# Performance work log

Hardware: AMD Instinct MI355X
Metric: run time of the kernel (lower is better)

The kernel has to match this reference:

```python
import jax, jax.numpy as jnp
import numpy as np

DIM = 2048
H = 16
DK = DIM // H   # head_k = 128
DV = DIM // H   # head_v = 128
B = 4
N = 4096
INV_SQRT_DK = 1.0 / float(np.sqrt(DK))


def setup_inputs() -> dict:
    key = jax.random.key(0)
    ks = jax.random.split(key, 12)
    s = 0.02
    return {
        "x": jax.random.normal(ks[0], (B, N, DIM), dtype=jnp.float32),
        "M_fast_prev": jax.random.normal(ks[1], (B, H, DK, DV), dtype=jnp.float32) * 0.05,
        "M_slow_prev": jax.random.normal(ks[2], (B, H, DK, DV), dtype=jnp.float32) * 0.05,
        "Wq": jax.random.normal(ks[3], (DIM, H * DK), dtype=jnp.float32) * s,
        "Wk": jax.random.normal(ks[4], (DIM, H * DK), dtype=jnp.float32) * s,
        "Wv": jax.random.normal(ks[5], (DIM, H * DV), dtype=jnp.float32) * s,
        "Wo": jax.random.normal(ks[6], (H * DV, DIM), dtype=jnp.float32) * s,
        "W_bilinear": jax.random.normal(ks[7], (H, DK, DK), dtype=jnp.float32) * 0.02,
        "fast_slope": jnp.full((H, 1, 1), 0.5, dtype=jnp.float32),
        "slow_slope": jnp.full((H, 1, 1), 0.01, dtype=jnp.float32),
        "inter_fast": jnp.full((H, 1, 1), 0.1, dtype=jnp.float32),
        "inter_slow": jnp.full((H, 1, 1), 0.9, dtype=jnp.float32),
        "S_fast": jax.random.normal(ks[8], (H, DK, DK), dtype=jnp.float32) * 0.05,
        "S_slow": jax.random.normal(ks[9], (H, DK, DK), dtype=jnp.float32) * 0.02,
        "f1_w": jax.random.normal(ks[10], (DIM, DIM // 2), dtype=jnp.float32) * s,
        "f1_b": jnp.zeros((DIM // 2,), dtype=jnp.float32),
        "f2_w": jax.random.normal(ks[11], (DIM // 2, H), dtype=jnp.float32) * s,
        "f2_b": jnp.zeros((H,), dtype=jnp.float32),
    }


def reference(x, M_fast_prev, M_slow_prev, Wq, Wk, Wv, Wo, W_bilinear,
              fast_slope, slow_slope, inter_fast, inter_slow,
              S_fast, S_slow, f1_w, f1_b, f2_w, f2_b):
    b, n, _ = x.shape
    # projections -> [b, h, n, d]
    q = (x @ Wq).reshape(b, n, H, DK).transpose(0, 2, 1, 3)
    k = (x @ Wk).reshape(b, n, H, DK).transpose(0, 2, 1, 3)
    v = (x @ Wv).reshape(b, n, H, DV).transpose(0, 2, 1, 3)

    # bilinear resonance modulation of keys
    resonance = jnp.tanh(jnp.einsum('bhnd,hde->bhne', k, W_bilinear))
    k_mod = k * (1.0 + 0.5 * resonance) * INV_SQRT_DK

    # exponential fast/slow decay weights over positions: [h, n, 1]
    idx = (jnp.arange(n, dtype=x.dtype) - (n - 1))[:, None]  # [n, 1]
    fast_w = jnp.exp(fast_slope * idx)  # [h, n, 1]
    slow_w = jnp.exp(slow_slope * idx)

    k_fast = k_mod * fast_w[None]  # [b, h, n, dk]
    k_slow = k_mod * slow_w[None]

    # outer-product state accumulation: [b, h, dk, dv]
    M_fast_curr = jnp.einsum('bhnd,bhnv->bhdv', k_fast, v)
    M_slow_curr = jnp.einsum('bhnd,bhnv->bhdv', k_slow, v)

    # inter-block state carry
    M_fast = M_fast_prev * inter_fast[None] + M_fast_curr
    M_slow = M_slow_prev * inter_slow[None] + M_slow_curr

    # refinement: (I + S) @ M
    eye = jnp.eye(DK, dtype=x.dtype)
    Mf_ref = jnp.einsum('hde,bhev->bhdv', eye[None] + S_fast, M_fast)
    Ms_ref = jnp.einsum('hde,bhev->bhdv', eye[None] + S_slow, M_slow)

    o_fast = jnp.einsum('bhnd,bhdv->bhnv', q, Mf_ref)
    o_slow = jnp.einsum('bhnd,bhdv->bhnv', q, Ms_ref)

    # flux gating from pooled tokens
    h1 = jax.nn.silu(x.mean(axis=1) @ f1_w + f1_b)
    psi = jax.nn.sigmoid(h1 @ f2_w + f2_b)  # [b, h]
    pe = psi[:, :, None, None]

    o_blend = (1.0 - pe) * o_fast + pe * o_slow  # [b, h, n, dv]
    o_blend = o_blend.transpose(0, 2, 1, 3).reshape(b, n, H * DV)
    out = o_blend @ Wo
    return out, M_fast, M_slow, psi
```

## Files before the change

kernel.cpp:

```cpp
#include <hip/hip_runtime.h>
#include <math.h>

typedef __bf16 bf16;
typedef __attribute__((ext_vector_type(8))) __bf16 bf16x8;
typedef __attribute__((ext_vector_type(4))) __bf16 bf16x4;
typedef __attribute__((ext_vector_type(2))) __bf16 bf16x2;
typedef __attribute__((ext_vector_type(4))) float f32x4;

#define DIM 2048
#define NH 16
#define DKK 128
#define BATCH 4
#define SEQ 4096
#define BN (BATCH*SEQ)
#define INV_SQRT_DK 0.08838834764831845f

#define MFMA16(a,b,c) __builtin_amdgcn_mfma_f32_16x16x32_bf16((a),(b),(c),0,0,0)

#define GLDS(gp, lp) __builtin_amdgcn_global_load_lds( \
    (const __attribute__((address_space(1))) void*)(gp), \
    (__attribute__((address_space(3))) void*)(lp), 16, 0, 0)

__device__ inline void stage_tile(const bf16* __restrict__ g, int ld,
                                  bf16* lds, int lane, int wave) {
  const int rl = lane >> 3;
  const int gc = ((lane & 7) ^ (rl & 7)) << 3;
  const bf16* gp = g + (size_t)(wave * 32 + rl) * ld + gc;
#pragma unroll
  for (int t = 0; t < 4; ++t)
    GLDS(gp + (size_t)(t * 8) * ld, lds + (wave * 32 + t * 8) * 64);
}

__device__ inline bf16x8 frag8(const bf16* lds, int r, int kc) {
  return *(const bf16x8*)(lds + r * 64 + (((kc ^ (r & 7)) << 3)));
}

__device__ inline int sq64(int r, int c) {
  return r * 64 + ((((c >> 3) ^ (r & 7)) << 3) | (c & 7));
}

__device__ inline float fast_exp(float x) { return __expf(x); }
__device__ inline float fast_tanh(float x) {
  float e2 = __expf(2.f * x);
  return 1.f - 2.f / (e2 + 1.f);
}

__global__ __launch_bounds__(256) void conv_bf16(const float* __restrict__ x,
                                                 bf16* __restrict__ y) {
  int i = (blockIdx.x * 256 + threadIdx.x) * 4;
  float4 v = *(const float4*)(x + i);
  bf16x4 o = { (bf16)v.x, (bf16)v.y, (bf16)v.z, (bf16)v.w };
  *(bf16x4*)(y + i) = o;
}

__global__ __launch_bounds__(256) void tconv3(const float* W0, const float* W1,
                                              const float* W2,
                                              bf16* O0, bf16* O1, bf16* O2) {
  __shared__ float tile[32][33];
  const float* Wp; bf16* Op;
  switch (blockIdx.z) {
    case 0: Wp = W0; Op = O0; break;
    case 1: Wp = W1; Op = O1; break;
    default: Wp = W2; Op = O2; break;
  }
  int c0 = blockIdx.x * 32, r0 = blockIdx.y * 32;
  int tx = threadIdx.x, ty = threadIdx.y;
#pragma unroll
  for (int i = 0; i < 4; ++i)
    tile[ty + i*8][tx] = Wp[(size_t)(r0 + ty + i*8) * DIM + c0 + tx];
  __syncthreads();
#pragma unroll
  for (int i = 0; i < 4; ++i)
    Op[(size_t)(c0 + ty + i*8) * DIM + r0 + tx] = (bf16)tile[tx][ty + i*8];
}

__global__ __launch_bounds__(256) void tconvWb(const float* __restrict__ W,
                                               bf16* __restrict__ Wt) {
  __shared__ float tile[32][33];
  const float* Wp = W + (size_t)blockIdx.z * DKK * DKK;
  bf16* Wtp = Wt + (size_t)blockIdx.z * DKK * DKK;
  int c0 = blockIdx.x * 32, r0 = blockIdx.y * 32;
  int tx = threadIdx.x, ty = threadIdx.y;
#pragma unroll
  for (int i = 0; i < 4; ++i)
    tile[ty + i*8][tx] = Wp[(size_t)(r0 + ty + i*8) * DKK + c0 + tx];
  __syncthreads();
#pragma unroll
  for (int i = 0; i < 4; ++i)
    Wtp[(size_t)(c0 + ty + i*8) * DKK + r0 + tx] = (bf16)tile[tx][ty + i*8];
}

__global__ __launch_bounds__(256) void rweights(const float* __restrict__ fs,
                                                const float* __restrict__ ss,
                                                float* __restrict__ rbuf) {
  int n = blockIdx.x * 256 + threadIdx.x;
  int h = blockIdx.y;
  rbuf[h * SEQ + n] = fast_exp((fs[h] - ss[h]) * (float)(n - (SEQ - 1)));
}

__global__ void zero_f32(float* p, int n) {
  int i = blockIdx.x * 256 + threadIdx.x;
  if (i < n) p[i] = 0.f;
}

__global__ __launch_bounds__(256) void mean_part(const bf16* __restrict__ xb,
                                                 float* __restrict__ xm) {
  int d0 = (blockIdx.x * 256 + threadIdx.x) * 2;
  int b = blockIdx.z;
  const bf16* xp = xb + ((size_t)b * SEQ + (size_t)blockIdx.y * 256) * DIM + d0;
  float s0 = 0.f, s1 = 0.f;
#pragma unroll 8
  for (int n = 0; n < 256; ++n) {
    bf16x2 v = *(const bf16x2*)(xp + (size_t)n * DIM);
    s0 += (float)v[0]; s1 += (float)v[1];
  }
  atomicAdd(&xm[b * DIM + d0], s0);
  atomicAdd(&xm[b * DIM + d0 + 1], s1);
}

__global__ __launch_bounds__(256) void mlp1(const float* __restrict__ xm,
                                            const float* __restrict__ f1w,
                                            float* __restrict__ h1raw) {
  int j = blockIdx.x * 256 + threadIdx.x;
  int b = blockIdx.y;
  int k0 = blockIdx.z * 256;
  const float* xmb = xm + b * DIM + k0;
  const float* w = f1w + (size_t)k0 * (DIM/2) + j;
  float s = 0.f;
#pragma unroll 4
  for (int k = 0; k < 256; ++k) s += xmb[k] * w[(size_t)k * (DIM/2)];
  atomicAdd(&h1raw[b * (DIM/2) + j], s);
}

__global__ void mlp2(const float* __restrict__ h1raw,
                     const float* __restrict__ f1b,
                     const float* __restrict__ f2w,
                     const float* __restrict__ f2b,
                     float* __restrict__ psi_out) {
  int t = threadIdx.x;
  int b = t >> 4, h = t & 15;
  float s = f2b[h];
  for (int k = 0; k < DIM/2; ++k) {
    float hv = h1raw[b * (DIM/2) + k] * (1.f / (float)SEQ) + f1b[k];
    hv = hv / (1.f + fast_exp(-hv));
    s += hv * f2w[k * NH + h];
  }
  psi_out[t] = 1.f / (1.f + fast_exp(-s));
}

template<int MODE>
__global__ __launch_bounds__(512, 2) void gemm256(const bf16* __restrict__ A, int lda,
                                                  const bf16* __restrict__ Bt, int ldb,
                                                  void* __restrict__ Cv, int ldc, int K) {
  __shared__ bf16 smem[65536];
  const int tid = threadIdx.x;
  const int lane = tid & 63;
  const int wave = tid >> 6;
  const int quad = lane >> 4;
  const int l15 = lane & 15;
  const int wm = (wave >> 2) * 128;
  const int wn = (wave & 3) * 64;
  const size_t m0 = (size_t)blockIdx.y * 256;
  const size_t n0 = (size_t)blockIdx.x * 256;
  const bf16* Ap = A;
  const bf16* Bp = Bt;
  size_t mrow = m0;
  size_t cbat = 0;
  if (MODE == 3) Bp += (size_t)(m0 >> 12) * DIM * DIM;
  if (MODE == 4) {
    size_t b = m0 >> 11;
    Ap += b * (size_t)DIM * DIM;
    cbat = b * (size_t)DIM * DIM;
    mrow = m0 & 2047;
  }
  const bf16* Arow = Ap + mrow * (size_t)lda;
  const bf16* Brow = Bp + n0 * (size_t)ldb;
  f32x4 acc[8][4] = {};
  const int NT = K >> 6;
  stage_tile(Arow, lda, smem, lane, wave);
  stage_tile(Brow, ldb, smem + 32768, lane, wave);
  for (int kt = 0; kt < NT; ++kt) {
    const int cur = kt & 1;
    const bf16* sA = smem + cur * 16384;
    const bf16* sB = smem + 32768 + cur * 16384;
    if (kt + 1 < NT) {
      const int nxt = cur ^ 1;
      const int k0 = (kt + 1) << 6;
      stage_tile(Arow + k0, lda, smem + nxt * 16384, lane, wave);
      stage_tile(Brow + k0, ldb, smem + 32768 + nxt * 16384, lane, wave);
      asm volatile("s_waitcnt vmcnt(8)\n\ts_barrier" ::: "memory");
    } else {
      asm volatile("s_waitcnt vmcnt(0)\n\ts_barrier" ::: "memory");
    }
    bf16x8 bfr[2][4];
#pragma unroll
    for (int kk = 0; kk < 2; ++kk)
#pragma unroll
      for (int j = 0; j < 4; ++j)
        bfr[kk][j] = frag8(sB, wn + j * 16 + l15, kk * 4 + quad);
#pragma unroll
    for (int i2 = 0; i2 < 4; ++i2) {
      bf16x8 af[2][2];
#pragma unroll
      for (int ii = 0; ii < 2; ++ii)
#pragma unroll
        for (int kk = 0; kk < 2; ++kk)
          af[ii][kk] = frag8(sA, wm + (i2 * 2 + ii) * 16 + l15, kk * 4 + quad);
      __builtin_amdgcn_s_setprio(1);
#pragma unroll
      for (int ii = 0; ii < 2; ++ii)
#pragma unroll
        for (int j = 0; j < 4; ++j) {
          acc[i2*2+ii][j] = MFMA16(af[ii][0], bfr[0][j], acc[i2*2+ii][j]);
          acc[i2*2+ii][j] = MFMA16(af[ii][1], bfr[1][j], acc[i2*2+ii][j]);
        }
      __builtin_amdgcn_s_setprio(0);
    }
    asm volatile("s_barrier" ::: "memory");
  }
  if (MODE == 2) {
    const int bb = (int)(m0 >> 12);
    const int nb0 = (int)(m0 & 4095) + wm + quad * 4;
    bf16* vt = (bf16*)Cv;
#pragma unroll
    for (int i = 0; i < 8; ++i)
#pragma unroll
      for (int j = 0; j < 4; ++j) {
        int colg = (int)n0 + wn + j * 16 + l15;
        int h = colg >> 7, dv = colg & 127;
        bf16x4 p = { (bf16)acc[i][j][0], (bf16)acc[i][j][1],
                     (bf16)acc[i][j][2], (bf16)acc[i][j][3] };
        *(bf16x4*)(vt + ((size_t)(bb * NH + h) * DKK + dv) * SEQ + nb0 + i * 16) = p;
      }
  } else {
#pragma unroll
    for (int i = 0; i < 8; ++i)
#pragma unroll
      for (int j = 0; j < 4; ++j) {
        size_t col = n0 + wn + j * 16 + l15;
        size_t row = mrow + wm + i * 16 + quad * 4;
#pragma unroll
        for (int r = 0; r < 4; ++r) {
          if (MODE == 3) ((float*)Cv)[(row + r) * ldc + col] = acc[i][j][r];
          else           ((bf16*)Cv)[cbat + (row + r) * ldc + col] = (bf16)acc[i][j][r];
        }
      }
  }
}

__global__ __launch_bounds__(256) void res_fuse(const bf16* __restrict__ kn,
                                                const bf16* __restrict__ Wbt,
                                                const float* __restrict__ slow_slope,
                                                bf16* __restrict__ kts) {
  __shared__ bf16 sA2[2][8192];
  __shared__ bf16 sB[8192];
  const int tid = threadIdx.x;
  const int lane = tid & 63;
  const int wave = tid >> 6;
  const int quad = lane >> 4;
  const int l15 = lane & 15;
  const int wm = (wave & 1) * 64;
  const int wn = (wave >> 1) * 64;
  const int nt = blockIdx.x;
  const int bh = blockIdx.y;
  const int h = bh & (NH - 1), b = bh >> 4;
  const bf16* Ap = kn + ((size_t)b * SEQ + (size_t)nt * 128) * DIM + h * DKK;
  const bf16* Bp = Wbt + (size_t)h * DKK * DKK;
  const float ss = slow_slope[h];
  f32x4 acc[4][4] = {};
#pragma unroll
  for (int c = 0; c < 2; ++c) {
    stage_tile(Ap + c * 64, DIM, sA2[c], lane, wave);
    stage_tile(Bp + c * 64, DKK, sB, lane, wave);
    __syncthreads();
#pragma unroll
    for (int kk = 0; kk < 2; ++kk) {
      const int kc = kk * 4 + quad;
      bf16x8 af[4], bfr[4];
#pragma unroll
      for (int i = 0; i < 4; ++i) af[i] = frag8(sA2[c], wm + i*16 + l15, kc);
#pragma unroll
      for (int j = 0; j < 4; ++j) bfr[j] = frag8(sB, wn + j*16 + l15, kc);
#pragma unroll
      for (int i = 0; i < 4; ++i)
#pragma unroll
        for (int j = 0; j < 4; ++j)
          acc[i][j] = MFMA16(af[i], bfr[j], acc[i][j]);
    }
    __syncthreads();
  }
  float wsv[4][4];
#pragma unroll
  for (int i = 0; i < 4; ++i)
#pragma unroll
    for (int r = 0; r < 4; ++r) {
      int ng = nt * 128 + wm + i*16 + quad*4 + r;
      wsv[i][r] = fast_exp(ss * (float)(ng - (SEQ - 1)));
    }
#pragma unroll
  for (int i = 0; i < 4; ++i)
#pragma unroll
    for (int j = 0; j < 4; ++j) {
      int e = wn + j*16 + l15;
      const bf16* sAe = sA2[e >> 6];
      int ec = e & 63;
      bf16x4 p;
#pragma unroll
      for (int r = 0; r < 4; ++r) {
        int nl = wm + i*16 + quad*4 + r;
        float kv = (float)sAe[sq64(nl, ec)];
        float res = fast_tanh(acc[i][j][r]);
        p[r] = (bf16)(kv * (1.f + 0.5f * res) * INV_SQRT_DK * wsv[i][r]);
      }
      *(bf16x4*)(kts + ((size_t)bh * DKK + e) * SEQ + nt * 128 + wm + i*16 + quad*4) = p;
    }
}

__global__ __launch_bounds__(256) void mcurr(const bf16* __restrict__ kts,
                                             const bf16* __restrict__ vt,
                                             const float* __restrict__ rbuf,
                                             float* __restrict__ partials) {
  __shared__ bf16 sK[128 * 64];
  __shared__ bf16 sV[128 * 64];
  const int tid = threadIdx.x;
  const int lane = tid & 63;
  const int wave = tid >> 6;
  const int quad = lane >> 4;
  const int wm = (wave & 1) * 64, wn = (wave >> 1) * 64;
  const int s = blockIdx.x;
  const int bh = blockIdx.y;
  const int h = bh & (NH - 1);
  const bf16* Ap = kts + (size_t)bh * DKK * SEQ;
  const bf16* Bp = vt + (size_t)bh * DKK * SEQ;
  const float* rp = rbuf + (size_t)h * SEQ;
  f32x4 accF[4][4] = {}, accS[4][4] = {};
  for (int k0 = s * 512; k0 < s * 512 + 512; k0 += 64) {
    stage_tile(Ap + k0, SEQ, sK, lane, wave);
    stage_tile(Bp + k0, SEQ, sV, lane, wave);
    __syncthreads();
#pragma unroll
    for (int kk = 0; kk < 2; ++kk) {
      const int kc = kk * 4 + quad;
      const int kn_ = k0 + kc * 8;
      float rv[8];
      *(f32x4*)rv       = *(const f32x4*)(rp + kn_);
      *(f32x4*)(rv + 4) = *(const f32x4*)(rp + kn_ + 4);
      bf16x8 afS[4], afF[4], bfv[4];
#pragma unroll
      for (int i = 0; i < 4; ++i) afS[i] = frag8(sK, wm + i*16 + (lane & 15), kc);
#pragma unroll
      for (int j = 0; j < 4; ++j) bfv[j] = frag8(sV, wn + j*16 + (lane & 15), kc);
#pragma unroll
      for (int i = 0; i < 4; ++i)
#pragma unroll
        for (int e = 0; e < 8; ++e)
          afF[i][e] = (bf16)((float)afS[i][e] * rv[e]);
#pragma unroll
      for (int i = 0; i < 4; ++i)
#pragma unroll
        for (int j = 0; j < 4; ++j) {
          accS[i][j] = MFMA16(afS[i], bfv[j], accS[i][j]);
          accF[i][j] = MFMA16(afF[i], bfv[j], accF[i][j]);
        }
    }
    __syncthreads();
  }
  float* Pf = partials + ((size_t)(s * 64 + bh) * 2 + 0) * (DKK * DKK);
  float* Ps = partials + ((size_t)(s * 64 + bh) * 2 + 1) * (DKK * DKK);
#pragma unroll
  for (int i = 0; i < 4; ++i)
#pragma unroll
    for (int j = 0; j < 4; ++j) {
      int col = wn + j*16 + (lane & 15);
      int row = wm + i*16 + quad * 4;
#pragma unroll
      for (int r = 0; r < 4; ++r) {
        Pf[(row + r) * DKK + col] = accF[i][j][r];
        Ps[(row + r) * DKK + col] = accS[i][j][r];
      }
    }
}

__global__ __launch_bounds__(256) void finalize(const float* __restrict__ partials,
                                                const float* __restrict__ Mf_prev,
                                                const float* __restrict__ Ms_prev,
                                                const float* __restrict__ inter_fast,
                                                const float* __restrict__ inter_slow,
                                                const float* __restrict__ S_fast,
                                                const float* __restrict__ S_slow,
                                                const float* __restrict__ psi,
                                                float* __restrict__ Mf_out,
                                                float* __restrict__ Ms_out,
                                                bf16* __restrict__ Mb) {
  __shared__ float sMf[128 * 33];
  __shared__ float sMs[128 * 33];
  const int t = threadIdx.x;
  const int bh = blockIdx.x;
  const int h = bh & (NH - 1);
  const int e0 = blockIdx.y * 32;
  const int el = t & 31;
  const int d0 = t >> 5;
  const float inf_ = inter_fast[h], ins_ = inter_slow[h];
  const size_t mb = (size_t)bh * (DKK * DKK);
#pragma unroll
  for (int i = 0; i < 16; ++i) {
    int d = d0 + 8 * i;
    int g = d * DKK + e0 + el;
    float mf = inf_ * Mf_prev[mb + g];
    float ms = ins_ * Ms_prev[mb + g];
#pragma unroll
    for (int s = 0; s < 8; ++s) {
      mf += partials[((size_t)(s * 64 + bh) * 2 + 0) * (DKK*DKK) + g];
      ms += partials[((size_t)(s * 64 + bh) * 2 + 1) * (DKK*DKK) + g];
    }
    Mf_out[mb + g] = mf;
    Ms_out[mb + g] = ms;
    sMf[d * 33 + el] = mf;
    sMs[d * 33 + el] = ms;
  }
  __syncthreads();
  const float p = psi[bh];
  for (int i = 0; i < 16; ++i) {
    int d = d0 + 8 * i;
    float accf = sMf[d * 33 + el];
    float accs = sMs[d * 33 + el];
    const float* Sf = S_fast + (size_t)h * (DKK*DKK) + (size_t)d * DKK;
    const float* Ss = S_slow + (size_t)h * (DKK*DKK) + (size_t)d * DKK;
    for (int k = 0; k < DKK; ++k) {
      accf += Sf[k] * sMf[k * 33 + el];
      accs += Ss[k] * sMs[k * 33 + el];
    }
    float blend = (1.f - p) * accf + p * accs;
    Mb[mb + (size_t)d * DKK + e0 + el] = (bf16)blend;
  }
}

__global__ __launch_bounds__(256) void w2_gemm(const bf16* __restrict__ Mb,
                                               const bf16* __restrict__ Wto,
                                               bf16* __restrict__ W2t) {
  __shared__ bf16 sA[128 * 64];
  __shared__ bf16 sB[128 * 64];
  const int tid = threadIdx.x;
  const int lane = tid & 63;
  const int wave = tid >> 6;
  const int quad = lane >> 4;
  const int wm = (wave & 1) * 64, wn = (wave >> 1) * 64;
  const int c0 = blockIdx.x * 128;
  const int bh = blockIdx.y;
  const int h = bh & (NH - 1), b = bh >> 4;
  const bf16* Ap = Mb + (size_t)bh * DKK * DKK;
  const bf16* Bp = Wto + (size_t)c0 * DIM + h * DKK;
  f32x4 acc[4][4] = {};
#pragma unroll
  for (int k0 = 0; k0 < DKK; k0 += 64) {
    stage_tile(Ap + k0, DKK, sA, lane, wave);
    stage_tile(Bp + k0, DIM, sB, lane, wave);
    __syncthreads();
#pragma unroll
    for (int kk = 0; kk < 2; ++kk) {
      const int kc = kk * 4 + quad;
      bf16x8 af[4], bfr[4];
#pragma unroll
      for (int i = 0; i < 4; ++i) af[i] = frag8(sA, wm + i*16 + (lane & 15), kc);
#pragma unroll
      for (int j = 0; j < 4; ++j) bfr[j] = frag8(sB, wn + j*16 + (lane & 15), kc);
#pragma unroll
      for (int i = 0; i < 4; ++i)
#pragma unroll
        for (int j = 0; j < 4; ++j)
          acc[i][j] = MFMA16(af[i], bfr[j], acc[i][j]);
    }
    __syncthreads();
  }
  bf16* base = W2t + (size_t)b * DIM * DIM + h * DKK;
#pragma unroll
  for (int i = 0; i < 4; ++i)
#pragma unroll
    for (int j = 0; j < 4; ++j) {
      int col = wn + j*16 + (lane & 15);
      int row0 = wm + i*16 + quad * 4;
      bf16x4 p = { (bf16)acc[i][j][0], (bf16)acc[i][j][1],
                   (bf16)acc[i][j][2], (bf16)acc[i][j][3] };
      *(bf16x4*)(base + (size_t)(c0 + col) * DIM + row0) = p;
    }
}

extern "C" void kernel_launch(void* const* d_in, const int* in_sizes, int n_in,
                              void* d_out, int out_size, void* d_ws, size_t ws_size,
                              hipStream_t stream) {
  const float* x        = (const float*)d_in[0];
  const float* Mf_prev  = (const float*)d_in[1];
  const float* Ms_prev  = (const float*)d_in[2];
  const float* Wq       = (const float*)d_in[3];
  const float* Wk       = (const float*)d_in[4];
  const float* Wv       = (const float*)d_in[5];
  const float* Wo       = (const float*)d_in[6];
  const float* Wbil     = (const float*)d_in[7];
  const float* fast_slope = (const float*)d_in[8];
  const float* slow_slope = (const float*)d_in[9];
  const float* inter_fast = (const float*)d_in[10];
  const float* inter_slow = (const float*)d_in[11];
  const float* S_fast   = (const float*)d_in[12];
  const float* S_slow   = (const float*)d_in[13];
  const float* f1w      = (const float*)d_in[14];
  const float* f1b      = (const float*)d_in[15];
  const float* f2w      = (const float*)d_in[16];
  const float* f2b      = (const float*)d_in[17];

  char* ws = (char*)d_ws;
  bf16*  xb       = (bf16*)(ws);
  bf16*  kn       = (bf16*)(ws + 67108864);
  float* partials = (float*)(ws + 67108864);
  bf16*  W2t      = (bf16*)(ws + 67108864);
  bf16*  Wcombt   = (bf16*)(ws + 100663296);
  bf16*  Wqb      = (bf16*)(ws + 134217728);
  bf16*  Wtk      = (bf16*)(ws + 142606336);
  bf16*  Wtv      = (bf16*)(ws + 150994944);
  bf16*  Wto      = (bf16*)(ws + 159383552);
  bf16*  Wbt      = (bf16*)(ws + 167772160);
  float* rbuf     = (float*)(ws + 168296448);
  bf16*  Mb       = (bf16*)(ws + 168558592);
  float* xm       = (float*)(ws + 170655744);
  float* h1raw    = (float*)(ws + 170688512);

  float* out  = (float*)d_out;
  float* MfO  = out + 33554432;
  float* MsO  = MfO + 1048576;
  float* psiO = MsO + 1048576;
  bf16* kts = (bf16*)d_out;
  bf16* vt  = kts + 33554432;

  conv_bf16<<<dim3(BN * DIM / 1024), 256, 0, stream>>>(x, xb);
  conv_bf16<<<dim3(DIM * DIM / 1024), 256, 0, stream>>>(Wq, Wqb);
  tconv3<<<dim3(64, 64, 3), dim3(32, 8), 0, stream>>>(Wk, Wv, Wo, Wtk, Wtv, Wto);
  tconvWb<<<dim3(4, 4, NH), dim3(32, 8), 0, stream>>>(Wbil, Wbt);
  rweights<<<dim3(16, 16), 256, 0, stream>>>(fast_slope, slow_slope, rbuf);

  zero_f32<<<dim3(48), 256, 0, stream>>>(xm, BATCH * DIM + BATCH * (DIM/2));
  mean_part<<<dim3(4, 16, 4), 256, 0, stream>>>(xb, xm);
  mlp1<<<dim3(4, 4, 8), 256, 0, stream>>>(xm, f1w, h1raw);
  mlp2<<<dim3(1), 64, 0, stream>>>(h1raw, f1b, f2w, f2b, psiO);

  gemm256<2><<<dim3(8, 64), 512, 0, stream>>>(xb, DIM, Wtv, DIM, vt, 0, DIM);
  gemm256<5><<<dim3(8, 64), 512, 0, stream>>>(xb, DIM, Wtk, DIM, kn, DIM, DIM);

  res_fuse<<<dim3(32, 64), 256, 0, stream>>>(kn, Wbt, slow_slope, kts);

  mcurr<<<dim3(8, 64), 256, 0, stream>>>(kts, vt, rbuf, partials);

  finalize<<<dim3(64, 4), 256, 0, stream>>>(partials, Mf_prev, Ms_prev, inter_fast,
                                            inter_slow, S_fast, S_slow, psiO,
                                            MfO, MsO, Mb);

  w2_gemm<<<dim3(16, 64), 256, 0, stream>>>(Mb, Wto, W2t);

  gemm256<4><<<dim3(8, 32), 512, 0, stream>>>(W2t, DIM, Wqb, DIM, Wcombt, DIM, DIM);

  gemm256<3><<<dim3(8, 64), 512, 0, stream>>>(xb, DIM, Wcombt, DIM, out, DIM, DIM);
}
```

Measured before the change: 1.138 ms.

## Restructure gemm256 into quadrant-ping-pong pipeline with half-tile staged loads

The 256x256 GEMM main loop is split into four quadrant sub-steps. Each sub-step loads one A or B half-tile fragment set from LDS, issues the global-to-LDS load for a future half-tile, then runs MFMAs on that quadrant. This interleaves memory traffic with compute at a finer grain and keeps prefetch two tiles deep, aiming to hide load latency. In exchange it adds more barriers per iteration, depends on a delicate vmcnt accounting, and changes the warp-to-output mapping to 2x2 quadrants of 64x32 sub-tiles.

```diff
diff --git a/kernel.cpp b/kernel.cpp
--- a/kernel.cpp
+++ b/kernel.cpp
@@ -20,6 +20,15 @@
 #define GLDS(gp, lp) __builtin_amdgcn_global_load_lds( \
     (const __attribute__((address_space(1))) void*)(gp), \
     (__attribute__((address_space(3))) void*)(lp), 16, 0, 0)
+
+__device__ inline void stage_half(const bf16* __restrict__ g, int ld,
+                                  bf16* lds, int lane, int wave) {
+  const int rl = lane >> 3;
+  const int gc = ((lane & 7) ^ (rl & 7)) << 3;
+  const bf16* gp = g + (size_t)(wave * 16 + rl) * ld + gc;
+  GLDS(gp,                  lds + (wave * 16) * 64);
+  GLDS(gp + (size_t)8 * ld, lds + (wave * 16 + 8) * 64);
+}
 
 __device__ inline void stage_tile(const bf16* __restrict__ g, int ld,
                                   bf16* lds, int lane, int wave) {
@@ -158,8 +167,8 @@
   const int wave = tid >> 6;
   const int quad = lane >> 4;
   const int l15 = lane & 15;
-  const int wm = (wave >> 2) * 128;
-  const int wn = (wave & 3) * 64;
+  const int wr2 = wave >> 2;
+  const int wc2 = wave & 3;
   const size_t m0 = (size_t)blockIdx.y * 256;
   const size_t n0 = (size_t)blockIdx.x * 256;
   const bf16* Ap = A;
@@ -175,76 +184,151 @@
   }
   const bf16* Arow = Ap + mrow * (size_t)lda;
   const bf16* Brow = Bp + n0 * (size_t)ldb;
-  f32x4 acc[8][4] = {};
   const int NT = K >> 6;
-  stage_tile(Arow, lda, smem, lane, wave);
-  stage_tile(Brow, ldb, smem + 32768, lane, wave);
-  for (int kt = 0; kt < NT; ++kt) {
-    const int cur = kt & 1;
+
+#define STA(tt, h) do { if ((tt) < NT) \
+    stage_half(Arow + (size_t)((h) * 128) * lda + (tt) * 64, lda, \
+               smem + ((tt) & 1) * 16384 + (h) * 8192, lane, wave); } while (0)
+#define STB(tt, h) do { if ((tt) < NT) \
+    stage_half(Brow + (size_t)((h) * 128) * ldb + (tt) * 64, ldb, \
+               smem + 32768 + ((tt) & 1) * 16384 + (h) * 8192, lane, wave); } while (0)
+#define WAIT_LGKM() do { \
+    asm volatile("s_waitcnt lgkmcnt(0)" ::: "memory"); \
+    __builtin_amdgcn_sched_barrier(0); } while (0)
+
+  f32x4 acc[2][2][4][2] = {};
+  STA(0, 0); STB(0, 0); STB(0, 1); STA(0, 1); STA(1, 0); STB(1, 1);
+  asm volatile("s_waitcnt vmcnt(4)\n\ts_barrier" ::: "memory");
+
+  for (int t = 0; t < NT; ++t) {
+    const int cur = t & 1;
     const bf16* sA = smem + cur * 16384;
     const bf16* sB = smem + 32768 + cur * 16384;
-    if (kt + 1 < NT) {
-      const int nxt = cur ^ 1;
-      const int k0 = (kt + 1) << 6;
-      stage_tile(Arow + k0, lda, smem + nxt * 16384, lane, wave);
-      stage_tile(Brow + k0, ldb, smem + 32768 + nxt * 16384, lane, wave);
-      asm volatile("s_waitcnt vmcnt(8)\n\ts_barrier" ::: "memory");
-    } else {
-      asm volatile("s_waitcnt vmcnt(0)\n\ts_barrier" ::: "memory");
-    }
-    bf16x8 bfr[2][4];
-#pragma unroll
-    for (int kk = 0; kk < 2; ++kk)
-#pragma unroll
-      for (int j = 0; j < 4; ++j)
-        bfr[kk][j] = frag8(sB, wn + j * 16 + l15, kk * 4 + quad);
-#pragma unroll
-    for (int i2 = 0; i2 < 4; ++i2) {
-      bf16x8 af[2][2];
-#pragma unroll
-      for (int ii = 0; ii < 2; ++ii)
-#pragma unroll
-        for (int kk = 0; kk < 2; ++kk)
-          af[ii][kk] = frag8(sA, wm + (i2 * 2 + ii) * 16 + l15, kk * 4 + quad);
-      __builtin_amdgcn_s_setprio(1);
-#pragma unroll
-      for (int ii = 0; ii < 2; ++ii)
-#pragma unroll
-        for (int j = 0; j < 4; ++j) {
-          acc[i2*2+ii][j] = MFMA16(af[ii][0], bfr[0][j], acc[i2*2+ii][j]);
-          acc[i2*2+ii][j] = MFMA16(af[ii][1], bfr[1][j], acc[i2*2+ii][j]);
-        }
-      __builtin_amdgcn_s_setprio(0);
-    }
-    asm volatile("s_barrier" ::: "memory");
-  }
+    bf16x8 a0[4][2], a1[4][2], b0[2][2], b1[2][2];
+
+#pragma unroll
+    for (int i = 0; i < 4; ++i)
+#pragma unroll
+      for (int kk = 0; kk < 2; ++kk)
+        a0[i][kk] = frag8(sA, wr2 * 64 + i * 16 + l15, kk * 4 + quad);
+#pragma unroll
+    for (int j = 0; j < 2; ++j)
+#pragma unroll
+      for (int kk = 0; kk < 2; ++kk)
+        b0[j][kk] = frag8(sB, wc2 * 32 + j * 16 + l15, kk * 4 + quad);
+    STA(t + 1, 1);
+    asm volatile("s_barrier" ::: "memory");
+    WAIT_LGKM();
+    __builtin_amdgcn_s_setprio(1);
+#pragma unroll
+    for (int i = 0; i < 4; ++i)
+#pragma unroll
+      for (int j = 0; j < 2; ++j) {
+        acc[0][0][i][j] = MFMA16(a0[i][0], b0[j][0], acc[0][0][i][j]);
+        acc[0][0][i][j] = MFMA16(a0[i][1], b0[j][1], acc[0][0][i][j]);
+      }
+    __builtin_amdgcn_s_setprio(0);
+    asm volatile("s_barrier" ::: "memory");
+
+#pragma unroll
+    for (int j = 0; j < 2; ++j)
+#pragma unroll
+      for (int kk = 0; kk < 2; ++kk)
+        b1[j][kk] = frag8(sB + 8192, wc2 * 32 + j * 16 + l15, kk * 4 + quad);
+    STB(t + 1, 0);
+    asm volatile("s_barrier" ::: "memory");
+    WAIT_LGKM();
+    __builtin_amdgcn_s_setprio(1);
+#pragma unroll
+    for (int i = 0; i < 4; ++i)
+#pragma unroll
+      for (int j = 0; j < 2; ++j) {
+        acc[0][1][i][j] = MFMA16(a0[i][0], b1[j][0], acc[0][1][i][j]);
+        acc[0][1][i][j] = MFMA16(a0[i][1], b1[j][1], acc[0][1][i][j]);
+      }
+    __builtin_amdgcn_s_setprio(0);
+    asm volatile("s_barrier" ::: "memory");
+
+#pragma unroll
+    for (int i = 0; i < 4; ++i)
+#pragma unroll
+      for (int kk = 0; kk < 2; ++kk)
+        a1[i][kk] = frag8(sA + 8192, wr2 * 64 + i * 16 + l15, kk * 4 + quad);
+    STA(t + 2, 0);
+    asm volatile("s_barrier" ::: "memory");
+    WAIT_LGKM();
+    __builtin_amdgcn_s_setprio(1);
+#pragma unroll
+    for (int i = 0; i < 4; ++i)
+#pragma unroll
+      for (int j = 0; j < 2; ++j) {
+        acc[1][1][i][j] = MFMA16(a1[i][0], b1[j][0], acc[1][1][i][j]);
+        acc[1][1][i][j] = MFMA16(a1[i][1], b1[j][1], acc[1][1][i][j]);
+      }
+    __builtin_amdgcn_s_setprio(0);
+    asm volatile("s_barrier" ::: "memory");
+
+#pragma unroll
+    for (int j = 0; j < 2; ++j)
+#pragma unroll
+      for (int kk = 0; kk < 2; ++kk)
+        b0[j][kk] = frag8(sB, wc2 * 32 + j * 16 + l15, kk * 4 + quad);
+    STB(t + 2, 1);
+    asm volatile("s_barrier" ::: "memory");
+    WAIT_LGKM();
+    __builtin_amdgcn_s_setprio(1);
+#pragma unroll
+    for (int i = 0; i < 4; ++i)
+#pragma unroll
+      for (int j = 0; j < 2; ++j) {
+        acc[1][0][i][j] = MFMA16(a1[i][0], b0[j][0], acc[1][0][i][j]);
+        acc[1][0][i][j] = MFMA16(a1[i][1], b0[j][1], acc[1][0][i][j]);
+      }
+    __builtin_amdgcn_s_setprio(0);
+    if (t < NT - 2)       asm volatile("s_waitcnt vmcnt(4)" ::: "memory");
+    else if (t == NT - 2) asm volatile("s_waitcnt vmcnt(0)" ::: "memory");
+    asm volatile("s_barrier" ::: "memory");
+  }
+#undef STA
+#undef STB
+#undef WAIT_LGKM
+
   if (MODE == 2) {
     const int bb = (int)(m0 >> 12);
-    const int nb0 = (int)(m0 & 4095) + wm + quad * 4;
     bf16* vt = (bf16*)Cv;
 #pragma unroll
-    for (int i = 0; i < 8; ++i)
-#pragma unroll
-      for (int j = 0; j < 4; ++j) {
-        int colg = (int)n0 + wn + j * 16 + l15;
-        int h = colg >> 7, dv = colg & 127;
-        bf16x4 p = { (bf16)acc[i][j][0], (bf16)acc[i][j][1],
-                     (bf16)acc[i][j][2], (bf16)acc[i][j][3] };
-        *(bf16x4*)(vt + ((size_t)(bb * NH + h) * DKK + dv) * SEQ + nb0 + i * 16) = p;
-      }
+    for (int qa = 0; qa < 2; ++qa)
+#pragma unroll
+      for (int qb = 0; qb < 2; ++qb)
+#pragma unroll
+        for (int i = 0; i < 4; ++i)
+#pragma unroll
+          for (int j = 0; j < 2; ++j) {
+            int colg = (int)n0 + qb * 128 + wc2 * 32 + j * 16 + l15;
+            int h = colg >> 7, dv = colg & 127;
+            int nb = (int)(m0 & 4095) + qa * 128 + wr2 * 64 + i * 16 + quad * 4;
+            f32x4 a = acc[qa][qb][i][j];
+            bf16x4 p = { (bf16)a[0], (bf16)a[1], (bf16)a[2], (bf16)a[3] };
+            *(bf16x4*)(vt + ((size_t)(bb * NH + h) * DKK + dv) * SEQ + nb) = p;
+          }
   } else {
 #pragma unroll
-    for (int i = 0; i < 8; ++i)
-#pragma unroll
-      for (int j = 0; j < 4; ++j) {
-        size_t col = n0 + wn + j * 16 + l15;
-        size_t row = mrow + wm + i * 16 + quad * 4;
-#pragma unroll
-        for (int r = 0; r < 4; ++r) {
-          if (MODE == 3) ((float*)Cv)[(row + r) * ldc + col] = acc[i][j][r];
-          else           ((bf16*)Cv)[cbat + (row + r) * ldc + col] = (bf16)acc[i][j][r];
-        }
-      }
+    for (int qa = 0; qa < 2; ++qa)
+#pragma unroll
+      for (int qb = 0; qb < 2; ++qb)
+#pragma unroll
+        for (int i = 0; i < 4; ++i)
+#pragma unroll
+          for (int j = 0; j < 2; ++j) {
+            size_t col = n0 + qb * 128 + wc2 * 32 + j * 16 + l15;
+            size_t row = mrow + qa * 128 + wr2 * 64 + i * 16 + quad * 4;
+            f32x4 a = acc[qa][qb][i][j];
+#pragma unroll
+            for (int r = 0; r < 4; ++r) {
+              if (MODE == 3) ((float*)Cv)[(row + r) * ldc + col] = a[r];
+              else           ((bf16*)Cv)[cbat + (row + r) * ldc + col] = (bf16)a[r];
+            }
+          }
   }
 }
 
```

Measured after the change: 1.131 ms. Within noise of the previous version (-0.6%).
